# Performance work log

Measured on AMD Instinct MI355X. Metric: run time of the kernel, lower is better.

Reference implementation:

```python
import jax, jax.numpy as jnp
import numpy as np

K, STRIDE, PAD = 3, 1, 1


def _unfold(x, k=K, stride=STRIDE, pad=PAD):
    # x: [B, C, H, W] -> patches [B, C*k*k, L] (im2col, torch nn.Unfold layout:
    # channel index = c*k*k + ki*k + kj)
    p = jax.lax.conv_general_dilated_patches(
        x, filter_shape=(k, k), window_strides=(stride, stride),
        padding=((pad, pad), (pad, pad)))  # [B, C*k*k, Ho, Wo]
    B = x.shape[0]
    return p.reshape(B, p.shape[1], -1)


def reference(x, weight, dweight, bias):
    B, C, H, W = x.shape
    O = weight.shape[0]
    cols = _unfold(x)                                   # [B, C*k*k, L]
    # scalar gate per spatial position: dweight . sigmoid(cols)
    gate = jnp.einsum('f,bfl->bl', dweight.reshape(-1), jax.nn.sigmoid(cols))
    gated = cols * gate[:, None, :]                     # [B, C*k*k, L]
    out = jnp.einsum('of,bfl->bol', weight.reshape(O, -1), gated)  # [B, O, L]
    out = out + bias[None, :, None]
    Ho, Wo = (H // 2, W // 2) if STRIDE == 2 else (H, W)
    return out.reshape(B, O, Ho, Wo)


def setup_inputs() -> dict:
    key = jax.random.key(0)
    k1, k2, k3, k4 = jax.random.split(key, 4)
    B, C, O, H, W = 8, 32, 32, 256, 256
    fan_out = O * K * K
    std = float(np.sqrt(2.0 / fan_out))
    return {
        'x': jax.random.normal(k1, (B, C, H, W), dtype=jnp.float32),
        'weight': jax.random.normal(k2, (O, C, K, K), dtype=jnp.float32) * std,
        'dweight': jax.random.normal(k3, (1, C, K, K), dtype=jnp.float32) * std,
        'bias': jax.random.normal(k4, (O,), dtype=jnp.float32),
    }
```

## Files before the change

### kernel.cpp

```cpp
#include <hip/hip_runtime.h>


typedef _Float16 half8 __attribute__((ext_vector_type(8)));
typedef _Float16 half4 __attribute__((ext_vector_type(4)));
typedef float f32x16 __attribute__((ext_vector_type(16)));

#define BATCH 8
#define CIN 32
#define COUT 32
#define HH 256
#define WW 256
#define TW 32
#define TH 8
#define HTW 34
#define HTH 10
#define CSTR 40
#define NCHUNK 18
#define NPOS (HTH*HTW)
#define NITEM (NPOS*8)

__global__ __launch_bounds__(256) void prep_pack(const float* __restrict__ w,
                                                 const float* __restrict__ dw,
                                                 _Float16* __restrict__ Apack,
                                                 _Float16* __restrict__ Adw) {
  int t = blockIdx.x * 256 + threadIdx.x;
  int tt = t < 9216 ? t : t - 9216;
  int q = tt >> 9, lane = (tt >> 3) & 63, j = tt & 7;
  int tap = q >> 1, h = q & 1;
  int o = lane & 31, lh = lane >> 5;
  int c = h * 16 + lh * 8 + j;
  if (t < 9216)
    Apack[t] = (_Float16)w[o * 288 + c * 9 + tap];
  else if (t < 18432)
    Adw[tt] = (_Float16)dw[c * 9 + tap];
}

__global__ __launch_bounds__(512, 4) void dynconv(
    const float* __restrict__ x, const _Float16* __restrict__ Apack,
    const _Float16* __restrict__ Adw, const float* __restrict__ bias,
    float* __restrict__ out) {
  __shared__ __align__(16) _Float16 lv[NPOS * CSTR];
  __shared__ __align__(16) _Float16 ls[NPOS * CSTR];

  const int bid = blockIdx.x;
  const int xt = bid & 7, yt = (bid >> 3) & 31, bb = bid >> 8;
  const int x0 = xt * TW, y0 = yt * TH;
  const int tid = threadIdx.x;

  for (int i = tid; i < NITEM; i += 512) {
    const int cg = i / NPOS;
    const int pos = i - cg * NPOS;
    const int yy = pos / HTW;
    const int xx = pos - yy * HTW;
    const int gy = y0 + yy - 1, gx = x0 + xx - 1;
    float v0 = 0.f, v1 = 0.f, v2 = 0.f, v3 = 0.f;
    if ((unsigned)gy < 256u && (unsigned)gx < 256u) {
      const float* xp = x + (((size_t)(bb * CIN + cg * 4)) << 16) + (gy << 8) + gx;
      v0 = xp[0]; v1 = xp[1 << 16]; v2 = xp[2 << 16]; v3 = xp[3 << 16];
    }
    const float s0 = __builtin_amdgcn_rcpf(1.f + __expf(-v0));
    const float s1 = __builtin_amdgcn_rcpf(1.f + __expf(-v1));
    const float s2 = __builtin_amdgcn_rcpf(1.f + __expf(-v2));
    const float s3 = __builtin_amdgcn_rcpf(1.f + __expf(-v3));
    half4 hv = {(_Float16)v0, (_Float16)v1, (_Float16)v2, (_Float16)v3};
    half4 hs = {(_Float16)s0, (_Float16)s1, (_Float16)s2, (_Float16)s3};
    *(half4*)(lv + pos * CSTR + cg * 4) = hv;
    *(half4*)(ls + pos * CSTR + cg * 4) = hs;
  }
  __syncthreads();

  const int lane = tid & 63, w8 = tid >> 6;
  const int ln = lane & 31, lh = lane >> 5;

  f32x16 acc, accg;
#pragma unroll
  for (int i = 0; i < 16; ++i) { acc[i] = 0.f; accg[i] = 0.f; }

#pragma unroll
  for (int q = 0; q < NCHUNK; ++q) {
    const int tap = q >> 1, h = q & 1;
    const int ki = tap / 3, kj = tap - ki * 3;
    const half8 a  = *(const half8*)(Apack + ((q * 64 + lane) << 3));
    const half8 ad = *(const half8*)(Adw   + ((q * 64 + lane) << 3));
    const int off = ((w8 + ki) * HTW + ln + kj) * CSTR + h * 16 + lh * 8;
    const half8 bv = *(const half8*)(lv + off);
    const half8 bs = *(const half8*)(ls + off);
    acc  = __builtin_amdgcn_mfma_f32_32x32x16_f16(a,  bv, acc,  0, 0, 0);
    accg = __builtin_amdgcn_mfma_f32_32x32x16_f16(ad, bs, accg, 0, 0, 0);
  }

  const int y = y0 + w8;
#pragma unroll
  for (int reg = 0; reg < 16; ++reg) {
    const int o = (reg & 3) + 8 * (reg >> 2) + 4 * lh;
    out[(((size_t)(bb * COUT + o)) << 16) + (y << 8) + x0 + ln] =
        acc[reg] * accg[reg] + bias[o];
  }
}

extern "C" void kernel_launch(void* const* d_in, const int* in_sizes, int n_in,
                              void* d_out, int out_size, void* d_ws, size_t ws_size,
                              hipStream_t stream) {
  const float* x    = (const float*)d_in[0];
  const float* wgt  = (const float*)d_in[1];
  const float* dw   = (const float*)d_in[2];
  const float* bias = (const float*)d_in[3];
  float* out = (float*)d_out;

  _Float16* Apack = (_Float16*)d_ws;
  _Float16* Adw   = Apack + 9216;

  prep_pack<<<(18432 + 255) / 256, 256, 0, stream>>>(wgt, dw, Apack, Adw);
  dynconv<<<BATCH * (HH / TH) * (WW / TW), 512, 0, stream>>>(x, Apack, Adw, bias, out);
}
```

Before: 144.4 us.

## Compute gate via scalar LDS atomic partial sums instead of a second MFMA

The per-position gate was previously computed by a redundant 32-row MFMA over a packed dweight matrix, with the sigmoid tile stored in a second fp16 LDS buffer. The gate is now accumulated in fp32 as per-tap partial sums in LDS using shared-memory atomics, then summed over the 3x3 neighbourhood per output pixel. This halves MFMA work and drops the sigmoid LDS tile. It also raises the occupancy hint and reorders block indexing so batch varies fastest. The trade-off is nine LDS atomics per staged item plus an extra zeroing pass and barrier.

```diff
diff --git a/kernel.cpp b/kernel.cpp
--- a/kernel.cpp
+++ b/kernel.cpp
@@ -3,6 +3,7 @@
 
 typedef _Float16 half8 __attribute__((ext_vector_type(8)));
 typedef _Float16 half4 __attribute__((ext_vector_type(4)));
+typedef float f32x4 __attribute__((ext_vector_type(4)));
 typedef float f32x16 __attribute__((ext_vector_type(16)));
 
 #define BATCH 8
@@ -22,30 +23,37 @@
 __global__ __launch_bounds__(256) void prep_pack(const float* __restrict__ w,
                                                  const float* __restrict__ dw,
                                                  _Float16* __restrict__ Apack,
-                                                 _Float16* __restrict__ Adw) {
+                                                 float* __restrict__ dwpack) {
   int t = blockIdx.x * 256 + threadIdx.x;
-  int tt = t < 9216 ? t : t - 9216;
-  int q = tt >> 9, lane = (tt >> 3) & 63, j = tt & 7;
-  int tap = q >> 1, h = q & 1;
-  int o = lane & 31, lh = lane >> 5;
-  int c = h * 16 + lh * 8 + j;
-  if (t < 9216)
+  if (t < 9216) {
+    int q = t >> 9, lane = (t >> 3) & 63, j = t & 7;
+    int tap = q >> 1, h = q & 1;
+    int o = lane & 31, lh = lane >> 5;
+    int c = h * 16 + lh * 8 + j;
     Apack[t] = (_Float16)w[o * 288 + c * 9 + tap];
-  else if (t < 18432)
-    Adw[tt] = (_Float16)dw[c * 9 + tap];
+  } else if (t < 9216 + 288) {
+    int i = t - 9216;
+    int cg = i / 36, r = i - cg * 36;
+    int tap = r >> 2, u = r & 3;
+    dwpack[i] = dw[(cg * 4 + u) * 9 + tap];
+  }
 }
 
-__global__ __launch_bounds__(512, 4) void dynconv(
+__global__ __launch_bounds__(512, 8) void dynconv(
     const float* __restrict__ x, const _Float16* __restrict__ Apack,
-    const _Float16* __restrict__ Adw, const float* __restrict__ bias,
+    const float* __restrict__ dwpack, const float* __restrict__ bias,
     float* __restrict__ out) {
   __shared__ __align__(16) _Float16 lv[NPOS * CSTR];
-  __shared__ __align__(16) _Float16 ls[NPOS * CSTR];
+  __shared__ float gpart[9 * NPOS];
 
-  const int bid = blockIdx.x;
-  const int xt = bid & 7, yt = (bid >> 3) & 31, bb = bid >> 8;
+  const int bid0 = blockIdx.x;
+  const int bb = bid0 & 7, idx = bid0 >> 3;
+  const int xt = idx & 7, yt = idx >> 3;
   const int x0 = xt * TW, y0 = yt * TH;
   const int tid = threadIdx.x;
+
+  for (int i = tid; i < 9 * NPOS; i += 512) gpart[i] = 0.f;
+  __syncthreads();
 
   for (int i = tid; i < NITEM; i += 512) {
     const int cg = i / NPOS;
@@ -63,30 +71,38 @@
     const float s2 = __builtin_amdgcn_rcpf(1.f + __expf(-v2));
     const float s3 = __builtin_amdgcn_rcpf(1.f + __expf(-v3));
     half4 hv = {(_Float16)v0, (_Float16)v1, (_Float16)v2, (_Float16)v3};
-    half4 hs = {(_Float16)s0, (_Float16)s1, (_Float16)s2, (_Float16)s3};
     *(half4*)(lv + pos * CSTR + cg * 4) = hv;
-    *(half4*)(ls + pos * CSTR + cg * 4) = hs;
+    const float* dwp = dwpack + cg * 36;
+#pragma unroll
+    for (int tap = 0; tap < 9; ++tap) {
+      const f32x4 d = *(const f32x4*)(dwp + tap * 4);
+      atomicAdd(&gpart[tap * NPOS + pos], d[0] * s0 + d[1] * s1 + d[2] * s2 + d[3] * s3);
+    }
   }
   __syncthreads();
 
   const int lane = tid & 63, w8 = tid >> 6;
   const int ln = lane & 31, lh = lane >> 5;
 
-  f32x16 acc, accg;
+  float gate = 0.f;
 #pragma unroll
-  for (int i = 0; i < 16; ++i) { acc[i] = 0.f; accg[i] = 0.f; }
+  for (int ki = 0; ki < 3; ++ki)
+#pragma unroll
+    for (int kj = 0; kj < 3; ++kj)
+      gate += gpart[(ki * 3 + kj) * NPOS + (w8 + ki) * HTW + ln + kj];
+
+  f32x16 acc;
+#pragma unroll
+  for (int i = 0; i < 16; ++i) acc[i] = 0.f;
 
 #pragma unroll
   for (int q = 0; q < NCHUNK; ++q) {
     const int tap = q >> 1, h = q & 1;
     const int ki = tap / 3, kj = tap - ki * 3;
-    const half8 a  = *(const half8*)(Apack + ((q * 64 + lane) << 3));
-    const half8 ad = *(const half8*)(Adw   + ((q * 64 + lane) << 3));
+    const half8 a = *(const half8*)(Apack + ((q * 64 + lane) << 3));
     const int off = ((w8 + ki) * HTW + ln + kj) * CSTR + h * 16 + lh * 8;
     const half8 bv = *(const half8*)(lv + off);
-    const half8 bs = *(const half8*)(ls + off);
-    acc  = __builtin_amdgcn_mfma_f32_32x32x16_f16(a,  bv, acc,  0, 0, 0);
-    accg = __builtin_amdgcn_mfma_f32_32x32x16_f16(ad, bs, accg, 0, 0, 0);
+    acc = __builtin_amdgcn_mfma_f32_32x32x16_f16(a, bv, acc, 0, 0, 0);
   }
 
   const int y = y0 + w8;
@@ -94,7 +110,7 @@
   for (int reg = 0; reg < 16; ++reg) {
     const int o = (reg & 3) + 8 * (reg >> 2) + 4 * lh;
     out[(((size_t)(bb * COUT + o)) << 16) + (y << 8) + x0 + ln] =
-        acc[reg] * accg[reg] + bias[o];
+        acc[reg] * gate + bias[o];
   }
 }
 
@@ -108,8 +124,8 @@
   float* out = (float*)d_out;
 
   _Float16* Apack = (_Float16*)d_ws;
-  _Float16* Adw   = Apack + 9216;
+  float* dwpack   = (float*)((char*)d_ws + 18432);
 
-  prep_pack<<<(18432 + 255) / 256, 256, 0, stream>>>(wgt, dw, Apack, Adw);
-  dynconv<<<BATCH * (HH / TH) * (WW / TW), 512, 0, stream>>>(x, Apack, Adw, bias, out);
+  prep_pack<<<(9216 + 288 + 255) / 256, 256, 0, stream>>>(wgt, dw, Apack, dwpack);
+  dynconv<<<BATCH * (HH / TH) * (WW / TW), 512, 0, stream>>>(x, Apack, dwpack, bias, out);
 }
```

New measurement: 356.2 us. 147% more time.
